# Performance work log

Measured on AMD Instinct MI355X. Metric: run time of the kernel, lower is better.

Reference implementation:

```python
import jax, jax.numpy as jnp
import numpy as np

NEG = -1e30  # log-space 'zero' that stays finite in fp32
EPS = 1e-7   # keras backend epsilon used by ctc_batch_cost


def _lse3(a, b, c):
    m = jnp.maximum(jnp.maximum(a, b), c)
    return m + jnp.log(jnp.exp(a - m) + jnp.exp(b - m) + jnp.exp(c - m))


def setup_inputs() -> dict:
    key = jax.random.key(0)
    k1, k2 = jax.random.split(key)
    B, T, C, U = 256, 1024, 128, 128
    logits = jax.random.normal(k1, (B, T, C), dtype=jnp.float32)
    y_pred = jax.nn.softmax(logits, axis=-1)  # ctc_batch_cost expects probabilities
    y_true = jax.random.randint(k2, (B, U), 0, C - 1)  # labels in [0, C-2]; blank = C-1
    return {"y_true": y_true, "y_pred": y_pred}


def reference(y_true, y_pred):
    # Faithful to tf.keras.backend.ctc_batch_cost with input_length = T,
    # label_length = U for every row; blank index = num_classes - 1.
    B, T, C = y_pred.shape
    U = y_true.shape[1]
    S = 2 * U + 1
    blank = C - 1

    logp = jnp.log(y_pred + EPS)  # [B, T, C]

    # Extended label sequence: blank, l1, blank, l2, ..., lU, blank
    ext = jnp.full((B, S), blank, dtype=y_true.dtype).at[:, 1::2].set(y_true)

    # Per-timestep log-probs of extended labels: [B, T, S]
    lp_ext = jnp.take_along_axis(logp, jnp.broadcast_to(ext[:, None, :], (B, T, S)), axis=2)

    # Skip transition s-2 -> s allowed iff ext[s] != blank and ext[s] != ext[s-2]
    allow = jnp.concatenate(
        [jnp.zeros((B, 2), bool), (ext[:, 2:] != blank) & (ext[:, 2:] != ext[:, :-2])],
        axis=1,
    )  # [B, S]

    alpha0 = (
        jnp.full((B, S), NEG, dtype=logp.dtype)
        .at[:, 0].set(lp_ext[:, 0, 0])
        .at[:, 1].set(lp_ext[:, 0, 1])
    )

    lp_t = jnp.moveaxis(lp_ext, 1, 0)  # [T, B, S]

    def step(alpha, lp):
        a1 = jnp.concatenate([jnp.full((B, 1), NEG, alpha.dtype), alpha[:, :-1]], axis=1)
        a2 = jnp.concatenate([jnp.full((B, 2), NEG, alpha.dtype), alpha[:, :-2]], axis=1)
        a2 = jnp.where(allow, a2, NEG)
        alpha = _lse3(alpha, a1, a2) + lp
        return alpha, None

    alphaT, _ = jax.lax.scan(step, alpha0, lp_t[1:])

    a, b = alphaT[:, S - 1], alphaT[:, S - 2]
    m = jnp.maximum(a, b)
    ll = m + jnp.log(jnp.exp(a - m) + jnp.exp(b - m))
    return (-ll)[:, None]  # [B, 1], matching ctc_batch_cost
```

## Files before the change

### kernel.cpp

```cpp
#include <hip/hip_runtime.h>
#include <math.h>


#define T_DIM 1024
#define C_DIM 128
#define U_DIM 128
#define LN2F  0.6931471805599453f

#define EPS_LIT "0x33d6bf95"

#define CMT(BP,BB) \
  "v_add_f32 v120, v124, " BB "\n\t" \
  "v_mov_b32 v121, v120\n\t" \
  "v_pk_add_f32 v[122:123], " BP ", v[124:125]\n\t"

#define ALPHA \
  "v_mov_b32_dpp v118, v115 wave_shr:1 row_mask:0xf bank_mask:0xf bound_ctrl:0\n\t" \
  "v_mov_b32 v119, v114\n\t" \
  "v_pk_add_f32 v[126:127], v[114:115], v[112:113]\n\t" \
  "v_pk_fma_f32 v[126:127], v[118:119], v[30:31], v[126:127]\n\t" \
  "v_pk_add_f32 v[112:113], v[112:113], v[118:119]\n\t" \
  "v_add_f32 v117, v115, v116\n\t" \
  "v_pk_mul_f32 v[114:115], v[126:127], v[122:123]\n\t" \
  "v_pk_mul_f32 v[112:113], v[112:113], v[120:121]\n\t" \
  "v_mul_f32 v116, v117, v120\n\t"

#define RENORM \
  "v_max_f32 v127, v112, v113\n\t" \
  "v_max_f32 v127, v127, v114\n\t" \
  "v_max_f32 v127, v127, v115\n\t" \
  "v_max_f32 v127, v127, v116\n\t" \
  "s_nop 1\n\t" \
  "v_max_f32_dpp v127, v127, v127 row_ror:8 row_mask:0xf bank_mask:0xf\n\t" \
  "s_nop 1\n\t" \
  "v_max_f32_dpp v127, v127, v127 row_ror:4 row_mask:0xf bank_mask:0xf\n\t" \
  "s_nop 1\n\t" \
  "v_max_f32_dpp v127, v127, v127 row_ror:2 row_mask:0xf bank_mask:0xf\n\t" \
  "s_nop 1\n\t" \
  "v_max_f32_dpp v127, v127, v127 row_ror:1 row_mask:0xf bank_mask:0xf\n\t" \
  "s_nop 1\n\t" \
  "v_readlane_b32 s91, v127, 0\n\t" \
  "v_readlane_b32 s92, v127, 16\n\t" \
  "v_readlane_b32 s93, v127, 32\n\t" \
  "v_readlane_b32 s94, v127, 48\n\t" \
  "s_nop 1\n\t" \
  "s_max_u32 s91, s91, s92\n\t" \
  "s_max_u32 s93, s93, s94\n\t" \
  "s_max_u32 s91, s91, s93\n\t" \
  "s_lshr_b32 s92, s91, 23\n\t" \
  "s_and_b32 s92, s92, 0xff\n\t" \
  "s_sub_u32 s93, 0x126, s92\n\t" \
  "s_min_u32 s93, s93, 0xfe\n\t" \
  "s_lshl_b32 s94, s93, 23\n\t" \
  "s_sub_u32 s95, 0x7f, s93\n\t" \
  "s_add_u32 %[EA], %[EA], s95\n\t" \
  "v_mul_f32 v112, s94, v112\n\t" \
  "v_mul_f32 v113, s94, v113\n\t" \
  "v_mul_f32 v114, s94, v114\n\t" \
  "v_mul_f32 v115, s94, v115\n\t" \
  "v_mul_f32 v116, s94, v116\n\t"

#define ST(...) ST_X(__VA_ARGS__)
#define ST_X(B0,B1,B2,BP,ROFF,RBOFF) \
  "s_waitcnt lgkmcnt(9)\n\t" \
  CMT(BP,B2) \
  "ds_read_b32 " B0 ", v12 offset:" ROFF "\n\t" \
  "ds_read_b32 " B1 ", v13 offset:" ROFF "\n\t" \
  "ds_read_b32 " B2 ", v14 offset:" RBOFF "\n\t" \
  ALPHA

#define K0 "v96","v97","v98","v[96:97]"
#define K1 "v100","v101","v102","v[100:101]"
#define K2 "v104","v105","v106","v[104:105]"
#define K3 "v108","v109","v110","v[108:109]"

#define PF(SL) \
  "global_load_dwordx4 v[" SL "], v10, %[P]\n\t" \
  "v_add_u32 v10, 0x400, v10\n\t"
#define PWL(SL,OFF) \
  "s_waitcnt vmcnt(15)\n\t" \
  "ds_write_b128 v11, v[" SL "] offset:" OFF "\n\t" \
  "global_load_dwordx4 v[" SL "], v10, %[P]\n\t" \
  "v_add_u32 v10, 0x400, v10\n\t"
#define PW(VC,SL,OFF) \
  "s_waitcnt vmcnt(" VC ")\n\t" \
  "ds_write_b128 v11, v[" SL "] offset:" OFF "\n\t"
#define PBAR \
  "s_waitcnt lgkmcnt(0)\n\t" \
  "s_barrier\n\t"

__global__ __launch_bounds__(128) void ctc_alpha_kernel(
    const int*   __restrict__ y_true,
    const float* __restrict__ y_pred,
    float*       __restrict__ out,
    int B)
{
  __shared__ float4 ldsbuf[1024];

  const int b = blockIdx.x;
  if (b >= B) return;
  const int tid  = threadIdx.x;
  const int lane = tid & 63;
  const int wid  = tid >> 6;
  const unsigned lds_off = (unsigned)(uintptr_t)(void*)ldsbuf;

  if (wid == 1) {
    const float* __restrict__ p = y_pred + (size_t)b * (T_DIM * C_DIM);
    const int gvoff  = lane * 16;
    const int wraddr = (int)lds_off + lane * 16;
    asm volatile(
      "s_mov_b32 m0, -1\n\t"
      "v_mov_b32 v10, %[GV]\n\t"
      "v_mov_b32 v11, %[WA]\n\t"
      PF("32:35") PF("36:39") PF("40:43") PF("44:47")
      PF("48:51") PF("52:55") PF("56:59") PF("60:63")
      PF("64:67") PF("68:71") PF("72:75") PF("76:79")
      PF("80:83") PF("84:87") PF("88:91") PF("92:95")
      PWL("32:35","0")    PWL("36:39","1024") PWL("40:43","2048") PWL("44:47","3072")
      PWL("48:51","4096") PWL("52:55","5120") PWL("56:59","6144") PWL("60:63","7168")
      PBAR
      "s_mov_b32 s90, 30\n"
      "LP_%=:\n\t"
      PBAR PWL("64:67","8192")  PWL("68:71","9216")  PWL("72:75","10240") PWL("76:79","11264")
      PBAR PWL("80:83","12288") PWL("84:87","13312") PWL("88:91","14336") PWL("92:95","15360")
      PBAR PWL("32:35","0")     PWL("36:39","1024")  PWL("40:43","2048")  PWL("44:47","3072")
      PBAR PWL("48:51","4096")  PWL("52:55","5120")  PWL("56:59","6144")  PWL("60:63","7168")
      "s_sub_u32 s90, s90, 1\n\t"
      "s_cmp_lg_u32 s90, 0\n\t"
      "s_cbranch_scc1 LP_%=\n\t"
      PBAR PWL("64:67","8192")  PWL("68:71","9216")  PWL("72:75","10240") PWL("76:79","11264")
      PBAR PWL("80:83","12288") PWL("84:87","13312") PWL("88:91","14336") PWL("92:95","15360")
      PBAR PW("15","32:35","0")     PW("14","36:39","1024")  PW("13","40:43","2048")  PW("12","44:47","3072")
      PBAR PW("11","48:51","4096")  PW("10","52:55","5120")  PW("9","56:59","6144")   PW("8","60:63","7168")
      PBAR PW("7","64:67","8192")   PW("6","68:71","9216")   PW("5","72:75","10240")  PW("4","76:79","11264")
      PBAR PW("3","80:83","12288")  PW("2","84:87","13312")  PW("1","88:91","14336")  PW("0","92:95","15360")
      PBAR
      PBAR
      :
      : [P]"s"(p), [GV]"v"(gvoff), [WA]"v"(wraddr)
      : "v10","v11",
        "v32","v33","v34","v35","v36","v37","v38","v39","v40","v41","v42","v43",
        "v44","v45","v46","v47","v48","v49","v50","v51","v52","v53","v54","v55",
        "v56","v57","v58","v59","v60","v61","v62","v63","v64","v65","v66","v67",
        "v68","v69","v70","v71","v72","v73","v74","v75","v76","v77","v78","v79",
        "v80","v81","v82","v83","v84","v85","v86","v87","v88","v89","v90","v91",
        "v92","v93","v94","v95",
        "s90","scc","memory");
    return;
  }

  const int* __restrict__ yb = y_true + b * U_DIM;
  const int blank = C_DIM - 1;
  const int ylab0 = yb[2 * lane];
  const int ylab1 = yb[2 * lane + 1];
  int yprev = blank;
  if (lane > 0) yprev = yb[2 * lane - 1];
  const float allow1 = (lane > 0 && ylab0 != blank && ylab0 != yprev) ? 1.0f : 0.0f;
  const float allow3 = (ylab1 != blank && ylab1 != ylab0)             ? 1.0f : 0.0f;

  const int rd1 = (int)lds_off + ylab0 * 4;
  const int rd3 = (int)lds_off + ylab1 * 4;
  const int rdb = (int)lds_off;

  const float init0 = (lane == 0) ? 1.0f : 0.0f;
  float a3out, a4out;
  int   e_acc = 0;

  asm volatile(
    "s_mov_b32 m0, -1\n\t"
    "v_mov_b32 v12, %[R1]\n\t"
    "v_mov_b32 v13, %[R3]\n\t"
    "v_mov_b32 v14, %[RB]\n\t"
    "v_mov_b32 v30, %[L1]\n\t"
    "v_mov_b32 v31, %[L3]\n\t"
    "v_mov_b32 v112, %[I0]\n\t"
    "v_mov_b32 v113, 0\n\t"
    "v_mov_b32 v114, 0\n\t"
    "v_mov_b32 v115, 0\n\t"
    "v_mov_b32 v116, 0\n\t"
    "v_mov_b32 v124, " EPS_LIT "\n\t"
    "v_mov_b32 v125, " EPS_LIT "\n\t"
    "s_barrier\n\t"
    "ds_read_b32 v96, v12 offset:0\n\t"
    "ds_read_b32 v97, v13 offset:0\n\t"
    "ds_read_b32 v98, v14 offset:508\n\t"
    "ds_read_b32 v100, v12 offset:512\n\t"
    "ds_read_b32 v101, v13 offset:512\n\t"
    "ds_read_b32 v102, v14 offset:1020\n\t"
    "ds_read_b32 v104, v12 offset:1024\n\t"
    "ds_read_b32 v105, v13 offset:1024\n\t"
    "ds_read_b32 v106, v14 offset:1532\n\t"
    "ds_read_b32 v108, v12 offset:1536\n\t"
    "ds_read_b32 v109, v13 offset:1536\n\t"
    "ds_read_b32 v110, v14 offset:2044\n\t"
    "s_mov_b32 s90, 32\n"
    "LM_%=:\n\t"
    "s_barrier\n\t"
    ST(K0,"2048","2556")   ST(K1,"2560","3068")   ST(K2,"3072","3580")   ST(K3,"3584","4092")
    ST(K0,"4096","4604")   ST(K1,"4608","5116")   ST(K2,"5120","5628")   ST(K3,"5632","6140")
    RENORM
    "s_barrier\n\t"
    ST(K0,"6144","6652")   ST(K1,"6656","7164")   ST(K2,"7168","7676")   ST(K3,"7680","8188")
    ST(K0,"8192","8700")   ST(K1,"8704","9212")   ST(K2,"9216","9724")   ST(K3,"9728","10236")
    RENORM
    "s_barrier\n\t"
    ST(K0,"10240","10748") ST(K1,"10752","11260") ST(K2,"11264","11772") ST(K3,"11776","12284")
    ST(K0,"12288","12796") ST(K1,"12800","13308") ST(K2,"13312","13820") ST(K3,"13824","14332")
    RENORM
    "s_barrier\n\t"
    ST(K0,"14336","14844") ST(K1,"14848","15356") ST(K2,"15360","15868") ST(K3,"15872","16380")
    ST(K0,"0","508")       ST(K1,"512","1020")    ST(K2,"1024","1532")   ST(K3,"1536","2044")
    RENORM
    "s_sub_u32 s90, s90, 1\n\t"
    "s_cmp_lg_u32 s90, 0\n\t"
    "s_cbranch_scc1 LM_%=\n\t"
    "s_waitcnt lgkmcnt(0)\n\t"
    "v_mov_b32 %[O3], v115\n\t"
    "v_mov_b32 %[O4], v116\n\t"
    : [O3]"=v"(a3out), [O4]"=v"(a4out), [EA]"+s"(e_acc)
    : [R1]"v"(rd1), [R3]"v"(rd3), [RB]"v"(rdb),
      [L1]"v"(allow1), [L3]"v"(allow3), [I0]"v"(init0)
    : "v12","v13","v14","v30","v31",
      "v96","v97","v98","v100","v101","v102",
      "v104","v105","v106","v108","v109","v110",
      "v112","v113","v114","v115","v116","v117","v118","v119","v120","v121",
      "v122","v123","v124","v125","v126","v127",
      "s90","s91","s92","s93","s94","s95","scc","memory");

  if (lane == 63) {
    float s = a3out + a4out;
    s = fmaxf(s, 1e-37f);
    float ll = logf(s) + (float)e_acc * LN2F;
    out[b] = -ll;
  }
}

extern "C" void kernel_launch(void* const* d_in, const int* in_sizes, int n_in,
                              void* d_out, int out_size, void* d_ws, size_t ws_size,
                              hipStream_t stream) {
  const int*   y_true = (const int*)d_in[0];
  const float* y_pred = (const float*)d_in[1];
  float*       out    = (float*)d_out;
  const int B = in_sizes[0] / U_DIM;
  ctc_alpha_kernel<<<dim3(B), dim3(128), 0, stream>>>(y_true, y_pred, out, B);
}
```

Measured before the change: 195.1 us.

## Split CTC alpha recursion across two waves with LDS handoff and producer-side epsilon add

The extended-label state range is split between two compute waves, so each lane now handles fewer states per step. Wave A handles the first half and publishes its boundary alpha and scale exponent through LDS; wave B lags one chunk behind, reads those values and rescales them into its own domain. The producer wave now adds epsilon to the probabilities before writing them to LDS, which takes that add off the serial recurrence. The cost is a third wave, a doubled LDS footprint, extra cross-wave exponent bookkeeping and pipeline skew between the two compute waves.

```diff
diff --git a/kernel.cpp b/kernel.cpp
--- a/kernel.cpp
+++ b/kernel.cpp
@@ -8,94 +8,147 @@
 #define LN2F  0.6931471805599453f
 
 #define EPS_LIT "0x33d6bf95"
-
-#define CMT(BP,BB) \
-  "v_add_f32 v120, v124, " BB "\n\t" \
-  "v_mov_b32 v121, v120\n\t" \
-  "v_pk_add_f32 v[122:123], " BP ", v[124:125]\n\t"
-
-#define ALPHA \
-  "v_mov_b32_dpp v118, v115 wave_shr:1 row_mask:0xf bank_mask:0xf bound_ctrl:0\n\t" \
-  "v_mov_b32 v119, v114\n\t" \
-  "v_pk_add_f32 v[126:127], v[114:115], v[112:113]\n\t" \
-  "v_pk_fma_f32 v[126:127], v[118:119], v[30:31], v[126:127]\n\t" \
-  "v_pk_add_f32 v[112:113], v[112:113], v[118:119]\n\t" \
-  "v_add_f32 v117, v115, v116\n\t" \
-  "v_pk_mul_f32 v[114:115], v[126:127], v[122:123]\n\t" \
-  "v_pk_mul_f32 v[112:113], v[112:113], v[120:121]\n\t" \
-  "v_mul_f32 v116, v117, v120\n\t"
-
-#define RENORM \
-  "v_max_f32 v127, v112, v113\n\t" \
-  "v_max_f32 v127, v127, v114\n\t" \
-  "v_max_f32 v127, v127, v115\n\t" \
-  "v_max_f32 v127, v127, v116\n\t" \
-  "s_nop 1\n\t" \
-  "v_max_f32_dpp v127, v127, v127 row_ror:8 row_mask:0xf bank_mask:0xf\n\t" \
-  "s_nop 1\n\t" \
-  "v_max_f32_dpp v127, v127, v127 row_ror:4 row_mask:0xf bank_mask:0xf\n\t" \
-  "s_nop 1\n\t" \
-  "v_max_f32_dpp v127, v127, v127 row_ror:2 row_mask:0xf bank_mask:0xf\n\t" \
-  "s_nop 1\n\t" \
-  "v_max_f32_dpp v127, v127, v127 row_ror:1 row_mask:0xf bank_mask:0xf\n\t" \
-  "s_nop 1\n\t" \
-  "v_readlane_b32 s91, v127, 0\n\t" \
-  "v_readlane_b32 s92, v127, 16\n\t" \
-  "v_readlane_b32 s93, v127, 32\n\t" \
-  "v_readlane_b32 s94, v127, 48\n\t" \
+#define ONE_LIT "0x3f800000"
+
+#define STA(...) STA_X(__VA_ARGS__)
+#define STA_X(C1,CB,RIMM,BIMM,HIMM) \
+  "v_mul_f32 v44, s80, v51\n\t" \
+  "ds_write_b32 v42, v44 offset:" HIMM "\n\t" \
+  "v_mov_b32_dpp v52, v51 wave_shr:1 row_mask:0xf bank_mask:0xf bound_ctrl:0\n\t" \
+  "v_add_f32 v53, v51, v50\n\t" \
+  "v_fma_f32 v53, v52, v45, v53\n\t" \
+  "v_add_f32 v50, v50, v52\n\t" \
+  "s_waitcnt lgkmcnt(9)\n\t" \
+  "v_mul_f32 v51, v53, " C1 "\n\t" \
+  "v_mul_f32 v50, v50, " CB "\n\t" \
+  "ds_read_b32 " C1 ", v40 offset:" RIMM "\n\t" \
+  "ds_read_b32 " CB ", v41 offset:" BIMM "\n\t"
+
+#define KA0 "v96","v97"
+#define KA1 "v98","v99"
+#define KA2 "v100","v101"
+#define KA3 "v102","v103"
+
+#define STB(...) STB_X(__VA_ARGS__)
+#define STB_X(H,C1,CB,RIMM,BIMM,HRIMM) \
+  "v_mov_b32_dpp v52, v51 wave_shr:1 row_mask:0xf bank_mask:0xf bound_ctrl:0\n\t" \
+  "s_waitcnt lgkmcnt(6)\n\t" \
+  "v_mul_f32 v44, s82, " H "\n\t" \
+  "v_cndmask_b32 v52, v52, v44, %[M]\n\t" \
+  "v_add_f32 v53, v51, v50\n\t" \
+  "v_fma_f32 v53, v52, v45, v53\n\t" \
+  "v_add_f32 v50, v50, v52\n\t" \
+  "v_add_f32 v55, v54, v51\n\t" \
+  "v_mul_f32 v51, v53, " C1 "\n\t" \
+  "v_mul_f32 v50, v50, " CB "\n\t" \
+  "v_mul_f32 v54, v55, " CB "\n\t" \
+  "ds_read_b32 " H ", v42 offset:" HRIMM "\n\t" \
+  "ds_read_b32 " C1 ", v40 offset:" RIMM "\n\t" \
+  "ds_read_b32 " CB ", v41 offset:" BIMM "\n\t"
+
+#define KB0 "v96","v97","v98"
+#define KB1 "v99","v100","v101"
+#define KB2 "v102","v103","v104"
+#define KB3 "v105","v106","v107"
+
+#define REDUCE60 \
+  "s_nop 1\n\t" \
+  "v_max_f32_dpp v60, v60, v60 row_ror:8 row_mask:0xf bank_mask:0xf\n\t" \
+  "s_nop 1\n\t" \
+  "v_max_f32_dpp v60, v60, v60 row_ror:4 row_mask:0xf bank_mask:0xf\n\t" \
+  "s_nop 1\n\t" \
+  "v_max_f32_dpp v60, v60, v60 row_ror:2 row_mask:0xf bank_mask:0xf\n\t" \
+  "s_nop 1\n\t" \
+  "v_max_f32_dpp v60, v60, v60 row_ror:1 row_mask:0xf bank_mask:0xf\n\t" \
+  "s_nop 1\n\t" \
+  "v_readlane_b32 s91, v60, 0\n\t" \
+  "v_readlane_b32 s92, v60, 16\n\t" \
+  "v_readlane_b32 s93, v60, 32\n\t" \
+  "v_readlane_b32 s94, v60, 48\n\t" \
   "s_nop 1\n\t" \
   "s_max_u32 s91, s91, s92\n\t" \
   "s_max_u32 s93, s93, s94\n\t" \
-  "s_max_u32 s91, s91, s93\n\t" \
+  "s_max_u32 s91, s91, s93\n\t"
+
+#define RENORM_A \
+  "v_max_f32 v60, v50, v51\n\t" \
+  REDUCE60 \
   "s_lshr_b32 s92, s91, 23\n\t" \
   "s_and_b32 s92, s92, 0xff\n\t" \
   "s_sub_u32 s93, 0x126, s92\n\t" \
   "s_min_u32 s93, s93, 0xfe\n\t" \
   "s_lshl_b32 s94, s93, 23\n\t" \
   "s_sub_u32 s95, 0x7f, s93\n\t" \
-  "s_add_u32 %[EA], %[EA], s95\n\t" \
-  "v_mul_f32 v112, s94, v112\n\t" \
-  "v_mul_f32 v113, s94, v113\n\t" \
-  "v_mul_f32 v114, s94, v114\n\t" \
-  "v_mul_f32 v115, s94, v115\n\t" \
-  "v_mul_f32 v116, s94, v116\n\t"
-
-#define ST(...) ST_X(__VA_ARGS__)
-#define ST_X(B0,B1,B2,BP,ROFF,RBOFF) \
-  "s_waitcnt lgkmcnt(9)\n\t" \
-  CMT(BP,B2) \
-  "ds_read_b32 " B0 ", v12 offset:" ROFF "\n\t" \
-  "ds_read_b32 " B1 ", v13 offset:" ROFF "\n\t" \
-  "ds_read_b32 " B2 ", v14 offset:" RBOFF "\n\t" \
-  ALPHA
-
-#define K0 "v96","v97","v98","v[96:97]"
-#define K1 "v100","v101","v102","v[100:101]"
-#define K2 "v104","v105","v106","v[104:105]"
-#define K3 "v108","v109","v110","v[108:109]"
+  "s_add_u32 s81, s81, s95\n\t" \
+  "s_sub_u32 s95, 0xfe, s93\n\t" \
+  "s_lshl_b32 s80, s95, 23\n\t" \
+  "v_mul_f32 v50, s94, v50\n\t" \
+  "v_mul_f32 v51, s94, v51\n\t"
+
+#define RENORM_B \
+  "v_max3_f32 v60, v50, v51, v54\n\t" \
+  REDUCE60 \
+  "s_lshr_b32 s92, s91, 23\n\t" \
+  "s_and_b32 s92, s92, 0xff\n\t" \
+  "s_mov_b32 s84, s92\n\t" \
+  "s_sub_u32 s93, 0x126, s92\n\t" \
+  "s_min_u32 s93, s93, 0xfe\n\t" \
+  "s_lshl_b32 s94, s93, 23\n\t" \
+  "s_cmp_lg_u32 s92, 0\n\t" \
+  "s_cselect_b32 s95, s93, 0x7f\n\t" \
+  "s_sub_u32 s95, 0x7f, s95\n\t" \
+  "s_add_u32 s81, s81, s95\n\t" \
+  "v_mul_f32 v50, s94, v50\n\t" \
+  "v_mul_f32 v51, s94, v51\n\t" \
+  "v_mul_f32 v54, s94, v54\n\t"
+
+#define FACTOR_B \
+  "v_readfirstlane_b32 s83, v24\n\t" \
+  "s_nop 1\n\t" \
+  "s_cmp_lg_u32 s84, 0\n\t" \
+  "s_cselect_b32 s81, s81, s83\n\t" \
+  "s_sub_i32 s85, s83, s81\n\t" \
+  "s_add_i32 s85, s85, 0x7f\n\t" \
+  "s_cmp_lt_i32 s85, 0\n\t" \
+  "s_cselect_b32 s85, 0, s85\n\t" \
+  "s_cmp_gt_i32 s85, 0xfe\n\t" \
+  "s_cselect_b32 s85, 0xfe, s85\n\t" \
+  "s_lshl_b32 s82, s85, 23\n\t"
+
+#define PUBA(GIMM) \
+  "v_mov_b32 v44, s81\n\t" \
+  "ds_write_b32 v43, v44 offset:" GIMM "\n\t"
+
+#define ENDA \
+  "s_waitcnt lgkmcnt(2)\n\t" \
+  "s_barrier\n\t"
 
 #define PF(SL) \
   "global_load_dwordx4 v[" SL "], v10, %[P]\n\t" \
   "v_add_u32 v10, 0x400, v10\n\t"
-#define PWL(SL,OFF) \
+#define PWLE(PA,PB,SL,OFF) \
   "s_waitcnt vmcnt(15)\n\t" \
+  "v_pk_add_f32 v[" PA "], v[" PA "], v[24:25]\n\t" \
+  "v_pk_add_f32 v[" PB "], v[" PB "], v[24:25]\n\t" \
   "ds_write_b128 v11, v[" SL "] offset:" OFF "\n\t" \
   "global_load_dwordx4 v[" SL "], v10, %[P]\n\t" \
   "v_add_u32 v10, 0x400, v10\n\t"
-#define PW(VC,SL,OFF) \
+#define PWE(VC,PA,PB,SL,OFF) \
   "s_waitcnt vmcnt(" VC ")\n\t" \
+  "v_pk_add_f32 v[" PA "], v[" PA "], v[24:25]\n\t" \
+  "v_pk_add_f32 v[" PB "], v[" PB "], v[24:25]\n\t" \
   "ds_write_b128 v11, v[" SL "] offset:" OFF "\n\t"
 #define PBAR \
   "s_waitcnt lgkmcnt(0)\n\t" \
   "s_barrier\n\t"
 
-__global__ __launch_bounds__(128) void ctc_alpha_kernel(
+__global__ __launch_bounds__(192) void ctc_alpha_kernel(
     const int*   __restrict__ y_true,
     const float* __restrict__ y_pred,
     float*       __restrict__ out,
     int B)
 {
-  __shared__ float4 ldsbuf[1024];
+  __shared__ float4 ldsbuf[2048];
 
   const int b = blockIdx.x;
   if (b >= B) return;
@@ -103,8 +156,9 @@
   const int lane = tid & 63;
   const int wid  = tid >> 6;
   const unsigned lds_off = (unsigned)(uintptr_t)(void*)ldsbuf;
-
-  if (wid == 1) {
+  const int blank = C_DIM - 1;
+
+  if (wid == 2) {
     const float* __restrict__ p = y_pred + (size_t)b * (T_DIM * C_DIM);
     const int gvoff  = lane * 16;
     const int wraddr = (int)lds_off + lane * 16;
@@ -112,33 +166,58 @@
       "s_mov_b32 m0, -1\n\t"
       "v_mov_b32 v10, %[GV]\n\t"
       "v_mov_b32 v11, %[WA]\n\t"
+      "v_mov_b32 v24, " EPS_LIT "\n\t"
+      "v_mov_b32 v25, " EPS_LIT "\n\t"
       PF("32:35") PF("36:39") PF("40:43") PF("44:47")
       PF("48:51") PF("52:55") PF("56:59") PF("60:63")
       PF("64:67") PF("68:71") PF("72:75") PF("76:79")
       PF("80:83") PF("84:87") PF("88:91") PF("92:95")
-      PWL("32:35","0")    PWL("36:39","1024") PWL("40:43","2048") PWL("44:47","3072")
-      PWL("48:51","4096") PWL("52:55","5120") PWL("56:59","6144") PWL("60:63","7168")
+      PWLE("32:33","34:35","32:35","0")    PWLE("36:37","38:39","36:39","1024")
+      PWLE("40:41","42:43","40:43","2048") PWLE("44:45","46:47","44:47","3072")
+      PWLE("48:49","50:51","48:51","4096") PWLE("52:53","54:55","52:55","5120")
+      PWLE("56:57","58:59","56:59","6144") PWLE("60:61","62:63","60:63","7168")
       PBAR
       "s_mov_b32 s90, 30\n"
       "LP_%=:\n\t"
-      PBAR PWL("64:67","8192")  PWL("68:71","9216")  PWL("72:75","10240") PWL("76:79","11264")
-      PBAR PWL("80:83","12288") PWL("84:87","13312") PWL("88:91","14336") PWL("92:95","15360")
-      PBAR PWL("32:35","0")     PWL("36:39","1024")  PWL("40:43","2048")  PWL("44:47","3072")
-      PBAR PWL("48:51","4096")  PWL("52:55","5120")  PWL("56:59","6144")  PWL("60:63","7168")
+      PWLE("64:65","66:67","64:67","8192")   PWLE("68:69","70:71","68:71","9216")
+      PWLE("72:73","74:75","72:75","10240")  PWLE("76:77","78:79","76:79","11264")
+      PBAR
+      PWLE("80:81","82:83","80:83","12288")  PWLE("84:85","86:87","84:87","13312")
+      PWLE("88:89","90:91","88:91","14336")  PWLE("92:93","94:95","92:95","15360")
+      PBAR
+      PWLE("32:33","34:35","32:35","0")      PWLE("36:37","38:39","36:39","1024")
+      PWLE("40:41","42:43","40:43","2048")   PWLE("44:45","46:47","44:47","3072")
+      PBAR
+      PWLE("48:49","50:51","48:51","4096")   PWLE("52:53","54:55","52:55","5120")
+      PWLE("56:57","58:59","56:59","6144")   PWLE("60:61","62:63","60:63","7168")
+      PBAR
       "s_sub_u32 s90, s90, 1\n\t"
       "s_cmp_lg_u32 s90, 0\n\t"
       "s_cbranch_scc1 LP_%=\n\t"
-      PBAR PWL("64:67","8192")  PWL("68:71","9216")  PWL("72:75","10240") PWL("76:79","11264")
-      PBAR PWL("80:83","12288") PWL("84:87","13312") PWL("88:91","14336") PWL("92:95","15360")
-      PBAR PW("15","32:35","0")     PW("14","36:39","1024")  PW("13","40:43","2048")  PW("12","44:47","3072")
-      PBAR PW("11","48:51","4096")  PW("10","52:55","5120")  PW("9","56:59","6144")   PW("8","60:63","7168")
-      PBAR PW("7","64:67","8192")   PW("6","68:71","9216")   PW("5","72:75","10240")  PW("4","76:79","11264")
-      PBAR PW("3","80:83","12288")  PW("2","84:87","13312")  PW("1","88:91","14336")  PW("0","92:95","15360")
+      PWLE("64:65","66:67","64:67","8192")   PWLE("68:69","70:71","68:71","9216")
+      PWLE("72:73","74:75","72:75","10240")  PWLE("76:77","78:79","76:79","11264")
+      PBAR
+      PWLE("80:81","82:83","80:83","12288")  PWLE("84:85","86:87","84:87","13312")
+      PWLE("88:89","90:91","88:91","14336")  PWLE("92:93","94:95","92:95","15360")
+      PBAR
+      PWE("15","32:33","34:35","32:35","0")     PWE("14","36:37","38:39","36:39","1024")
+      PWE("13","40:41","42:43","40:43","2048")  PWE("12","44:45","46:47","44:47","3072")
+      PBAR
+      PWE("11","48:49","50:51","48:51","4096")  PWE("10","52:53","54:55","52:55","5120")
+      PWE("9","56:57","58:59","56:59","6144")   PWE("8","60:61","62:63","60:63","7168")
+      PBAR
+      PWE("7","64:65","66:67","64:67","8192")   PWE("6","68:69","70:71","68:71","9216")
+      PWE("5","72:73","74:75","72:75","10240")  PWE("4","76:77","78:79","76:79","11264")
+      PBAR
+      PWE("3","80:81","82:83","80:83","12288")  PWE("2","84:85","86:87","84:87","13312")
+      PWE("1","88:89","90:91","88:91","14336")  PWE("0","92:93","94:95","92:95","15360")
+      PBAR
+      PBAR
       PBAR
       PBAR
       :
       : [P]"s"(p), [GV]"v"(gvoff), [WA]"v"(wraddr)
-      : "v10","v11",
+      : "v10","v11","v24","v25",
         "v32","v33","v34","v35","v36","v37","v38","v39","v40","v41","v42","v43",
         "v44","v45","v46","v47","v48","v49","v50","v51","v52","v53","v54","v55",
         "v56","v57","v58","v59","v60","v61","v62","v63","v64","v65","v66","v67",
@@ -150,85 +229,173 @@
   }
 
   const int* __restrict__ yb = y_true + b * U_DIM;
-  const int blank = C_DIM - 1;
-  const int ylab0 = yb[2 * lane];
-  const int ylab1 = yb[2 * lane + 1];
-  int yprev = blank;
-  if (lane > 0) yprev = yb[2 * lane - 1];
-  const float allow1 = (lane > 0 && ylab0 != blank && ylab0 != yprev) ? 1.0f : 0.0f;
-  const float allow3 = (ylab1 != blank && ylab1 != ylab0)             ? 1.0f : 0.0f;
-
-  const int rd1 = (int)lds_off + ylab0 * 4;
-  const int rd3 = (int)lds_off + ylab1 * 4;
-  const int rdb = (int)lds_off;
-
-  const float init0 = (lane == 0) ? 1.0f : 0.0f;
-  float a3out, a4out;
+
+  if (wid == 0) {
+    const int ylab = yb[lane];
+    int yprev = blank;
+    if (lane > 0) yprev = yb[lane - 1];
+    const float allowA = (lane > 0 && ylab != blank && ylab != yprev) ? 1.0f : 0.0f;
+    const int rdC1 = (int)lds_off + ylab * 4;
+    const int rdCB = (int)lds_off;
+    const int hwA  = (int)lds_off + ((lane == 63) ? 16384 : (20608 + lane * 4));
+    const int ewA  = (int)lds_off + ((lane == 63) ? 24704 : (25216 + lane * 4));
+    const float init0 = (lane == 0) ? 1.0f : 0.0f;
+
+    asm volatile(
+      "s_mov_b32 m0, -1\n\t"
+      "v_mov_b32 v40, %[RC]\n\t"
+      "v_mov_b32 v41, %[RB]\n\t"
+      "v_mov_b32 v42, %[HW]\n\t"
+      "v_mov_b32 v43, %[EW]\n\t"
+      "v_mov_b32 v45, %[L]\n\t"
+      "v_mov_b32 v50, %[I0]\n\t"
+      "v_mov_b32 v51, 0\n\t"
+      "s_mov_b32 s80, " ONE_LIT "\n\t"
+      "s_mov_b32 s81, 0\n\t"
+      "s_barrier\n\t"
+      "ds_read_b32 v96, v40 offset:0\n\t"
+      "ds_read_b32 v97, v41 offset:508\n\t"
+      "ds_read_b32 v32, v41 offset:0\n\t"
+      "ds_read_b32 v32, v41 offset:0\n\t"
+      "ds_read_b32 v98, v40 offset:512\n\t"
+      "ds_read_b32 v99, v41 offset:1020\n\t"
+      "ds_read_b32 v32, v41 offset:0\n\t"
+      "ds_read_b32 v100, v40 offset:1024\n\t"
+      "ds_read_b32 v101, v41 offset:1532\n\t"
+      "ds_read_b32 v102, v40 offset:1536\n\t"
+      "ds_read_b32 v103, v41 offset:2044\n\t"
+      "s_mov_b32 s90, 32\n"
+      "LA_%=:\n\t"
+      PUBA("0")
+      STA(KA0,"2048","2556","0")   STA(KA1,"2560","3068","4")
+      STA(KA2,"3072","3580","8")   STA(KA3,"3584","4092","12")
+      STA(KA0,"4096","4604","16")  STA(KA1,"4608","5116","20")
+      STA(KA2,"5120","5628","24")  STA(KA3,"5632","6140","28")
+      RENORM_A ENDA
+      PUBA("4")
+      STA(KA0,"6144","6652","32")  STA(KA1,"6656","7164","36")
+      STA(KA2,"7168","7676","40")  STA(KA3,"7680","8188","44")
+      STA(KA0,"8192","8700","48")  STA(KA1,"8704","9212","52")
+      STA(KA2,"9216","9724","56")  STA(KA3,"9728","10236","60")
+      RENORM_A ENDA
+      PUBA("8")
+      STA(KA0,"10240","10748","64") STA(KA1,"10752","11260","68")
+      STA(KA2,"11264","11772","72") STA(KA3,"11776","12284","76")
+      STA(KA0,"12288","12796","80") STA(KA1,"12800","13308","84")
+      STA(KA2,"13312","13820","88") STA(KA3,"13824","14332","92")
+      RENORM_A ENDA
+      PUBA("12")
+      STA(KA0,"14336","14844","96")  STA(KA1,"14848","15356","100")
+      STA(KA2,"15360","15868","104") STA(KA3,"15872","16380","108")
+      STA(KA0,"0","508","112")       STA(KA1,"512","1020","116")
+      STA(KA2,"1024","1532","120")   STA(KA3,"1536","2044","124")
+      RENORM_A ENDA
+      "v_add_u32 v42, 128, v42\n\t"
+      "v_add_u32 v43, 16, v43\n\t"
+      "s_sub_u32 s90, s90, 1\n\t"
+      "s_cmp_lg_u32 s90, 0\n\t"
+      "s_cbranch_scc1 LA_%=\n\t"
+      "s_barrier\n\t"
+      "s_waitcnt lgkmcnt(0)\n\t"
+      :
+      : [RC]"v"(rdC1), [RB]"v"(rdCB), [HW]"v"(hwA), [EW]"v"(ewA),
+        [L]"v"(allowA), [I0]"v"(init0)
+      : "v32","v40","v41","v42","v43","v44","v45","v50","v51","v52","v53",
+        "v60","v96","v97","v98","v99","v100","v101","v102","v103",
+        "s80","s81","s90","s91","s92","s93","s94","s95","scc","memory");
+    return;
+  }
+
+  const int ylab = yb[64 + lane];
+  const int yprev = yb[63 + lane];
+  const float allowB = (ylab != blank && ylab != yprev) ? 1.0f : 0.0f;
+  const int rdC1 = (int)lds_off + ylab * 4;
+  const int rdCB = (int)lds_off;
+  const int hrB  = (int)lds_off + 16384;
+  const int erB  = (int)lds_off + 24704;
+  const unsigned long long mask0 = 1ULL;
+  float a1out, a4out;
   int   e_acc = 0;
 
   asm volatile(
     "s_mov_b32 m0, -1\n\t"
-    "v_mov_b32 v12, %[R1]\n\t"
-    "v_mov_b32 v13, %[R3]\n\t"
-    "v_mov_b32 v14, %[RB]\n\t"
-    "v_mov_b32 v30, %[L1]\n\t"
-    "v_mov_b32 v31, %[L3]\n\t"
-    "v_mov_b32 v112, %[I0]\n\t"
-    "v_mov_b32 v113, 0\n\t"
-    "v_mov_b32 v114, 0\n\t"
-    "v_mov_b32 v115, 0\n\t"
-    "v_mov_b32 v116, 0\n\t"
-    "v_mov_b32 v124, " EPS_LIT "\n\t"
-    "v_mov_b32 v125, " EPS_LIT "\n\t"
-    "s_barrier\n\t"
-    "ds_read_b32 v96, v12 offset:0\n\t"
-    "ds_read_b32 v97, v13 offset:0\n\t"
-    "ds_read_b32 v98, v14 offset:508\n\t"
-    "ds_read_b32 v100, v12 offset:512\n\t"
-    "ds_read_b32 v101, v13 offset:512\n\t"
-    "ds_read_b32 v102, v14 offset:1020\n\t"
-    "ds_read_b32 v104, v12 offset:1024\n\t"
-    "ds_read_b32 v105, v13 offset:1024\n\t"
-    "ds_read_b32 v106, v14 offset:1532\n\t"
-    "ds_read_b32 v108, v12 offset:1536\n\t"
-    "ds_read_b32 v109, v13 offset:1536\n\t"
-    "ds_read_b32 v110, v14 offset:2044\n\t"
+    "v_mov_b32 v40, %[RC]\n\t"
+    "v_mov_b32 v41, %[RB]\n\t"
+    "v_mov_b32 v42, %[HR]\n\t"
+    "v_mov_b32 v43, %[ER]\n\t"
+    "v_mov_b32 v45, %[L]\n\t"
+    "v_mov_b32 v50, 0\n\t"
+    "v_mov_b32 v51, 0\n\t"
+    "v_mov_b32 v54, 0\n\t"
+    "s_mov_b32 s82, " ONE_LIT "\n\t"
+    "s_mov_b32 s81, 0\n\t"
+    "s_barrier\n\t"
+    "s_barrier\n\t"
+    "ds_read_b32 v97, v40 offset:0\n\t"
+    "ds_read_b32 v98, v41 offset:508\n\t"
+    "ds_read_b32 v96, v42 offset:0\n\t"
+    "ds_read_b32 v32, v41 offset:0\n\t"
+    "ds_read_b32 v32, v41 offset:0\n\t"
+    "ds_read_b32 v100, v40 offset:512\n\t"
+    "ds_read_b32 v101, v41 offset:1020\n\t"
+    "ds_read_b32 v99, v42 offset:4\n\t"
+    "ds_read_b32 v32, v41 offset:0\n\t"
+    "ds_read_b32 v103, v40 offset:1024\n\t"
+    "ds_read_b32 v104, v41 offset:1532\n\t"
+    "ds_read_b32 v102, v42 offset:8\n\t"
+    "ds_read_b32 v106, v40 offset:1536\n\t"
+    "ds_read_b32 v107, v41 offset:2044\n\t"
+    "ds_read_b32 v105, v42 offset:12\n\t"
     "s_mov_b32 s90, 32\n"
-    "LM_%=:\n\t"
-    "s_barrier\n\t"
-    ST(K0,"2048","2556")   ST(K1,"2560","3068")   ST(K2,"3072","3580")   ST(K3,"3584","4092")
-    ST(K0,"4096","4604")   ST(K1,"4608","5116")   ST(K2,"5120","5628")   ST(K3,"5632","6140")
-    RENORM
-    "s_barrier\n\t"
-    ST(K0,"6144","6652")   ST(K1,"6656","7164")   ST(K2,"7168","7676")   ST(K3,"7680","8188")
-    ST(K0,"8192","8700")   ST(K1,"8704","9212")   ST(K2,"9216","9724")   ST(K3,"9728","10236")
-    RENORM
-    "s_barrier\n\t"
-    ST(K0,"10240","10748") ST(K1,"10752","11260") ST(K2,"11264","11772") ST(K3,"11776","12284")
-    ST(K0,"12288","12796") ST(K1,"12800","13308") ST(K2,"13312","13820") ST(K3,"13824","14332")
-    RENORM
-    "s_barrier\n\t"
-    ST(K0,"14336","14844") ST(K1,"14848","15356") ST(K2,"15360","15868") ST(K3,"15872","16380")
-    ST(K0,"0","508")       ST(K1,"512","1020")    ST(K2,"1024","1532")   ST(K3,"1536","2044")
-    RENORM
+    "LB_%=:\n\t"
+    "ds_read_b32 v24, v43 offset:0\n\t"
+    STB(KB0,"2048","2556","16")  STB(KB1,"2560","3068","20")
+    STB(KB2,"3072","3580","24")  STB(KB3,"3584","4092","28")
+    STB(KB0,"4096","4604","32")  STB(KB1,"4608","5116","36")
+    STB(KB2,"5120","5628","40")  STB(KB3,"5632","6140","44")
+    RENORM_B FACTOR_B
+    "s_barrier\n\t"
+    "ds_read_b32 v24, v43 offset:4\n\t"
+    STB(KB0,"6144","6652","48")  STB(KB1,"6656","7164","52")
+    STB(KB2,"7168","7676","56")  STB(KB3,"7680","8188","60")
+    STB(KB0,"8192","8700","64")  STB(KB1,"8704","9212","68")
+    STB(KB2,"9216","9724","72")  STB(KB3,"9728","10236","76")
+    RENORM_B FACTOR_B
+    "s_barrier\n\t"
+    "ds_read_b32 v24, v43 offset:8\n\t"
+    STB(KB0,"10240","10748","80") STB(KB1,"10752","11260","84")
+    STB(KB2,"11264","11772","88") STB(KB3,"11776","12284","92")
+    STB(KB0,"12288","12796","96") STB(KB1,"12800","13308","100")
+    STB(KB2,"13312","13820","104") STB(KB3,"13824","14332","108")
+    RENORM_B FACTOR_B
+    "s_barrier\n\t"
+    "ds_read_b32 v24, v43 offset:12\n\t"
+    STB(KB0,"14336","14844","112") STB(KB1,"14848","15356","116")
+    STB(KB2,"15360","15868","120") STB(KB3,"15872","16380","124")
+    "v_add_u32 v42, 128, v42\n\t"
+    STB(KB0,"0","508","0")        STB(KB1,"512","1020","4")
+    STB(KB2,"1024","1532","8")    STB(KB3,"1536","2044","12")
+    RENORM_B FACTOR_B
+    "s_barrier\n\t"
+    "v_add_u32 v43, 16, v43\n\t"
     "s_sub_u32 s90, s90, 1\n\t"
     "s_cmp_lg_u32 s90, 0\n\t"
-    "s_cbranch_scc1 LM_%=\n\t"
+    "s_cbranch_scc1 LB_%=\n\t"
     "s_waitcnt lgkmcnt(0)\n\t"
-    "v_mov_b32 %[O3], v115\n\t"
-    "v_mov_b32 %[O4], v116\n\t"
-    : [O3]"=v"(a3out), [O4]"=v"(a4out), [EA]"+s"(e_acc)
-    : [R1]"v"(rd1), [R3]"v"(rd3), [RB]"v"(rdb),
-      [L1]"v"(allow1), [L3]"v"(allow3), [I0]"v"(init0)
-    : "v12","v13","v14","v30","v31",
-      "v96","v97","v98","v100","v101","v102",
-      "v104","v105","v106","v108","v109","v110",
-      "v112","v113","v114","v115","v116","v117","v118","v119","v120","v121",
-      "v122","v123","v124","v125","v126","v127",
-      "s90","s91","s92","s93","s94","s95","scc","memory");
+    "v_mov_b32 %[O3], v51\n\t"
+    "v_mov_b32 %[O4], v54\n\t"
+    "s_mov_b32 %[EA], s81\n\t"
+    : [O3]"=v"(a1out), [O4]"=v"(a4out), [EA]"=s"(e_acc)
+    : [RC]"v"(rdC1), [RB]"v"(rdCB), [HR]"v"(hrB), [ER]"v"(erB),
+      [L]"v"(allowB), [M]"s"(mask0)
+    : "v24","v32","v40","v41","v42","v43","v44","v45","v50","v51","v52","v53",
+      "v54","v55","v60","v96","v97","v98","v99","v100","v101","v102","v103",
+      "v104","v105","v106","v107",
+      "s80","s81","s82","s83","s84","s85","s90","s91","s92","s93","s94","s95",
+      "scc","memory");
 
   if (lane == 63) {
-    float s = a3out + a4out;
+    float s = a1out + a4out;
     s = fmaxf(s, 1e-37f);
     float ll = logf(s) + (float)e_acc * LN2F;
     out[b] = -ll;
@@ -242,5 +409,5 @@
   const float* y_pred = (const float*)d_in[1];
   float*       out    = (float*)d_out;
   const int B = in_sizes[0] / U_DIM;
-  ctc_alpha_kernel<<<dim3(B), dim3(128), 0, stream>>>(y_true, y_pred, out, B);
+  ctc_alpha_kernel<<<dim3(B), dim3(192), 0, stream>>>(y_true, y_pred, out, B);
 }
```

After: 195.3 us. Within noise of the previous version (+0.1%).
